# Optimization experiments

Hardware: AMD Instinct MI355X
Metric: run time of the kernel (lower is better)

The kernel has to match this reference:

```python
import jax, jax.numpy as jnp
import numpy as np
from jax import lax

T, B = 256, 64
VOCAB, EMB, HID, NLAB = 100000, 300, 256, 20
PAD_WORD = 0


def setup_inputs() -> dict:
    key = jax.random.key(0)
    ks = jax.random.split(key, 16)
    sentences = jax.random.randint(ks[0], (T, B), 0, VOCAB)
    sentences = sentences.at[0].set(jnp.maximum(sentences[0], 1))  # mask[0] must be all on (torchcrf)
    labels = jax.random.randint(ks[1], (T, B), 0, NLAB)
    s = 0.05
    emb = jax.random.normal(ks[2], (VOCAB, EMB), jnp.float32) * s
    Wih_f = jax.random.normal(ks[3], (4 * HID, EMB), jnp.float32) * s
    Whh_f = jax.random.normal(ks[4], (4 * HID, HID), jnp.float32) * s
    b_f = jax.random.normal(ks[5], (4 * HID,), jnp.float32) * s
    Wih_b = jax.random.normal(ks[6], (4 * HID, EMB), jnp.float32) * s
    Whh_b = jax.random.normal(ks[7], (4 * HID, HID), jnp.float32) * s
    b_b = jax.random.normal(ks[8], (4 * HID,), jnp.float32) * s
    W_top = jax.random.normal(ks[9], (NLAB, 2 * HID), jnp.float32) * s
    b_top = jax.random.normal(ks[10], (NLAB,), jnp.float32) * s
    start_t = jax.random.normal(ks[11], (NLAB,), jnp.float32) * 0.1
    end_t = jax.random.normal(ks[12], (NLAB,), jnp.float32) * 0.1
    trans = jax.random.normal(ks[13], (NLAB, NLAB), jnp.float32) * 0.1
    return dict(emb=emb, Wih_f=Wih_f, Whh_f=Whh_f, b_f=b_f, Wih_b=Wih_b,
                Whh_b=Whh_b, b_b=b_b, W_top=W_top, b_top=b_top,
                start_t=start_t, end_t=end_t, trans=trans,
                sentences=sentences, labels=labels)


def _lstm_dir(x, W_ih, W_hh, b, reverse):
    # x: (T, B, E) -> hs: (T, B, H); torch gate order i,f,g,o
    H = W_hh.shape[1]
    x_proj = jnp.einsum('tbe,ge->tbg', x, W_ih) + b  # precompute input projection

    def step(carry, xp):
        h, c = carry
        gates = xp + h @ W_hh.T
        i, f, g, o = jnp.split(gates, 4, axis=-1)
        c = jax.nn.sigmoid(f) * c + jax.nn.sigmoid(i) * jnp.tanh(g)
        h = jax.nn.sigmoid(o) * jnp.tanh(c)
        return (h, c), h

    init = (jnp.zeros((x.shape[1], H), x.dtype), jnp.zeros((x.shape[1], H), x.dtype))
    _, hs = lax.scan(step, init, x_proj, reverse=reverse)
    return hs


def _crf_nll(emissions, tags, mask, start_t, end_t, trans):
    # emissions: (T,B,L), tags: (T,B), mask: (T,B) bool. torchcrf math, reduction='sum'.
    Tn, Bn, L = emissions.shape
    maskf = mask.astype(emissions.dtype)
    barange = jnp.arange(Bn)
    # numerator
    score = start_t[tags[0]] + emissions[0, barange, tags[0]]
    trans_sc = trans[tags[:-1], tags[1:]]  # (T-1, B)
    emit_sc = jnp.take_along_axis(emissions[1:], tags[1:, :, None], axis=2)[..., 0]
    score = score + ((trans_sc + emit_sc) * maskf[1:]).sum(0)
    seq_ends = mask.astype(jnp.int32).sum(0) - 1  # (B,)
    last_tags = jnp.take_along_axis(tags, seq_ends[None, :], axis=0)[0]
    score = score + end_t[last_tags]
    # partition (log-sum-exp forward recurrence)
    alpha0 = start_t[None, :] + emissions[0]  # (B, L)

    def step(alpha, inp):
        emis_t, m_t = inp
        nxt = jax.nn.logsumexp(alpha[:, :, None] + trans[None] + emis_t[:, None, :], axis=1)
        return jnp.where(m_t[:, None], nxt, alpha), None

    alpha, _ = lax.scan(step, alpha0, (emissions[1:], mask[1:]))
    denom = jax.nn.logsumexp(alpha + end_t[None, :], axis=1)
    llh = (score - denom).sum()
    return -llh


def reference(emb, Wih_f, Whh_f, b_f, Wih_b, Whh_b, b_b, W_top, b_top,
              start_t, end_t, trans, sentences, labels):
    x = emb[sentences]  # (T, B, E)
    h_f = _lstm_dir(x, Wih_f, Whh_f, b_f, reverse=False)
    h_b = _lstm_dir(x, Wih_b, Whh_b, b_b, reverse=True)
    rnn_out = jnp.concatenate([h_f, h_b], axis=-1)  # (T, B, 2H)
    emissions = jnp.einsum('tbh,lh->tbl', rnn_out, W_top) + b_top
    mask = sentences != PAD_WORD
    return _crf_nll(emissions, labels, mask, start_t, end_t, trans)
```

## Files before the change

### kernel.cpp

```cpp
#include <hip/hip_runtime.h>
#include <hip/hip_bf16.h>

#define T_    256
#define B_    64
#define EMB_  300
#define HID_  256
#define G_    1024
#define L_    20
#define M_    (T_*B_)

#define NCL   32
#define CLB   8
#define BPC   4
#define UPB   32

typedef float f32x4 __attribute__((ext_vector_type(4)));
typedef unsigned long long u64;

__global__ __launch_bounds__(256) void k_xproj(
    const float* __restrict__ emb,
    const float* __restrict__ Wih_f, const float* __restrict__ b_f,
    const float* __restrict__ Wih_b, const float* __restrict__ b_b,
    const int*   __restrict__ sent,
    float* __restrict__ xp)
{
    __shared__ float As[16][68];
    __shared__ float Bs[16][68];
    __shared__ int   words[64];

    const int tid = threadIdx.x;
    const int n0  = blockIdx.x * 64;
    const int m0  = blockIdx.y * 64;
    const int dir = n0 >> 10;
    const int g0  = n0 & 1023;
    const float* __restrict__ Wih  = dir ? Wih_b : Wih_f;
    const float* __restrict__ bias = dir ? b_b   : b_f;

    if (tid < 64) words[tid] = sent[m0 + tid];
    __syncthreads();

    const int r = tid >> 2;
    const int q = tid & 3;
    const float* aptr = emb + (size_t)words[r] * EMB_ + q * 4;
    const float* bptr = Wih + (size_t)(g0 + r) * EMB_ + q * 4;

    const int tx = tid & 15;
    const int ty = tid >> 4;
    float acc[4][4] = {};

    for (int k0 = 0; k0 < 304; k0 += 16) {
        const int k = k0 + q * 4;
        float4 av = make_float4(0.f, 0.f, 0.f, 0.f);
        float4 bv = make_float4(0.f, 0.f, 0.f, 0.f);
        if (k < 300) {
            av = *(const float4*)(aptr + k0);
            bv = *(const float4*)(bptr + k0);
        }
        As[q*4+0][r] = av.x; As[q*4+1][r] = av.y; As[q*4+2][r] = av.z; As[q*4+3][r] = av.w;
        Bs[q*4+0][r] = bv.x; Bs[q*4+1][r] = bv.y; Bs[q*4+2][r] = bv.z; Bs[q*4+3][r] = bv.w;
        __syncthreads();
        #pragma unroll
        for (int kk = 0; kk < 16; ++kk) {
            const float4 a = *(const float4*)&As[kk][ty * 4];
            const float4 b = *(const float4*)&Bs[kk][tx * 4];
            acc[0][0] += a.x*b.x; acc[0][1] += a.x*b.y; acc[0][2] += a.x*b.z; acc[0][3] += a.x*b.w;
            acc[1][0] += a.y*b.x; acc[1][1] += a.y*b.y; acc[1][2] += a.y*b.z; acc[1][3] += a.y*b.w;
            acc[2][0] += a.z*b.x; acc[2][1] += a.z*b.y; acc[2][2] += a.z*b.z; acc[2][3] += a.z*b.w;
            acc[3][0] += a.w*b.x; acc[3][1] += a.w*b.y; acc[3][2] += a.w*b.z; acc[3][3] += a.w*b.w;
        }
        __syncthreads();
    }

    float* out = xp + (size_t)dir * M_ * G_;
    const int g = g0 + tx * 4;
    const float4 bs4 = *(const float4*)(bias + g);
    #pragma unroll
    for (int im = 0; im < 4; ++im) {
        const int m = m0 + ty * 4 + im;
        float4 rv;
        rv.x = acc[im][0] + bs4.x;
        rv.y = acc[im][1] + bs4.y;
        rv.z = acc[im][2] + bs4.z;
        rv.w = acc[im][3] + bs4.w;
        *(float4*)(out + (size_t)m * G_ + g) = rv;
    }
}

__global__ __launch_bounds__(256, 1) void k_lstm_scan(
    const float* __restrict__ Whh_f, const float* __restrict__ Whh_b,
    const float* __restrict__ xp, float* __restrict__ hbuf,
    u64* __restrict__ xch)
{
    const int rank = blockIdx.x & 7;
    const int cl   = blockIdx.x >> 3;
    const int dir  = cl >> 4;
    const int bg   = cl & 15;
    const int b0   = bg * BPC;
    const int u0   = rank * UPB;
    const int tid  = threadIdx.x;
    const int lane = tid & 63;
    const int w    = tid >> 6;
    const int kh   = lane & 1;
    const int g    = (lane >> 1) & 3;
    const int u_loc = (w << 3) | (lane >> 3);

    const float* __restrict__ Whh = dir ? Whh_b : Whh_f;
    const float* __restrict__ xpd = xp + (size_t)dir * M_ * G_;
    float* __restrict__ hdir = hbuf + (size_t)dir * M_ * HID_;
    u64* __restrict__ xc = xch + (size_t)cl * 2048;

    __shared__ float hs[2][BPC][264];

    for (int i = tid; i < BPC * 264; i += 256) ((float*)hs[0])[i] = 0.f;

    f32x4 wv[32];
    {
        const f32x4* wrow = (const f32x4*)(Whh + (size_t)(g * HID_ + u0 + u_loc) * HID_ + kh * 128);
        #pragma unroll
        for (int i = 0; i < 32; ++i) wv[i] = wrow[i];
    }
    __syncthreads();

    float c_reg = 0.f;
    u64 vv[4] = {0ull, 0ull, 0ull, 0ull};

    for (int t = 0; t < T_; ++t) {
        const int t_eff = dir ? (T_ - 1 - t) : t;

        #pragma unroll
        for (int i = 0; i < 32; ++i) asm volatile("" : "+v"(wv[i]));

        float x0 = 0.f, x1 = 0.f, x2 = 0.f, x3 = 0.f;
        if (kh == 0) {
            const float* xrow = xpd + ((size_t)t_eff * B_ + (b0 + g)) * G_ + (u0 + u_loc);
            x0 = xrow[0]; x1 = xrow[HID_]; x2 = xrow[2 * HID_]; x3 = xrow[3 * HID_];
        }

        u64* const slot_cur = xc + (size_t)(t & 1) * 1024;
        u64* const slot_nxt = xc + (size_t)((t + 1) & 1) * 1024;
        float* const hcur = (float*)hs[t & 1];

        #pragma unroll
        for (int b = 0; b < 4; ++b) {
            {
                const int wn = (b + 2) & 3;
                u64* const sp = (b >= 2) ? slot_nxt : slot_cur;
                vv[wn] = __hip_atomic_load(&sp[(size_t)wn * 256 + tid],
                                           __ATOMIC_RELAXED, __HIP_MEMORY_SCOPE_AGENT);
            }

            if (t > 0) {
                const unsigned want = (unsigned)t;
                u64 v = vv[b];
                while ((unsigned)(v >> 32) != want)
                    v = __hip_atomic_load(&slot_cur[(size_t)b * 256 + tid],
                                          __ATOMIC_RELAXED, __HIP_MEMORY_SCOPE_AGENT);
                hcur[b * 264 + (tid >> 7) * 132 + (tid & 127)] =
                    __uint_as_float((unsigned)v);
            }
            __syncthreads();

            const f32x4* hv = (const f32x4*)(hcur + b * 264 + kh * 132);
            float acc = 0.f;
            #pragma unroll
            for (int i = 0; i < 32; ++i) {
                const f32x4 w4 = wv[i];
                const f32x4 h4 = hv[i];
                acc += w4.x * h4.x + w4.y * h4.y + w4.z * h4.z + w4.w * h4.w;
            }
            acc += __shfl_xor(acc, 1);

            const float v1 = __shfl_xor(acc, 2);
            const float v2 = __shfl_xor(acc, 4);
            const float v3 = __shfl_xor(v1, 4);

            if (g == b && kh == 0) {
                const float arr[4] = {acc, v1, v2, v3};
                const float gi = arr[b ^ 0] + x0;
                const float gf = arr[b ^ 1] + x1;
                const float gg = arr[b ^ 2] + x2;
                const float go = arr[b ^ 3] + x3;
                const float i_ = 1.f / (1.f + __expf(-gi));
                const float f_ = 1.f / (1.f + __expf(-gf));
                const float g_ = tanhf(gg);
                const float o_ = 1.f / (1.f + __expf(-go));
                const float cn = f_ * c_reg + i_ * g_;
                const float hn = o_ * tanhf(cn);
                c_reg = cn;
                if (t + 1 < T_) {
                    const u64 pkv = ((u64)(unsigned)(t + 1) << 32) | __float_as_uint(hn);
                    __hip_atomic_store(&slot_nxt[(size_t)b * 256 + (u0 + u_loc)], pkv,
                                       __ATOMIC_RELAXED, __HIP_MEMORY_SCOPE_AGENT);
                }
                hdir[((size_t)t_eff * B_ + (b0 + b)) * HID_ + (u0 + u_loc)] = hn;
            }
        }
    }
}

__global__ __launch_bounds__(256) void k_emis(
    const float* __restrict__ Wt, const float* __restrict__ bt,
    const float* __restrict__ hbuf, float* __restrict__ em)
{
    const int gid = blockIdx.x * 256 + threadIdx.x;
    if (gid >= M_ * L_) return;
    const int m = gid / L_;
    const int l = gid - m * L_;
    const float4* hf  = (const float4*)(hbuf + (size_t)m * HID_);
    const float4* hbk = (const float4*)(hbuf + (size_t)M_ * HID_ + (size_t)m * HID_);
    const float4* w0  = (const float4*)(Wt + (size_t)l * 2 * HID_);
    const float4* w1  = w0 + HID_ / 4;
    float acc = bt[l];
    #pragma unroll 4
    for (int k = 0; k < HID_ / 4; ++k) {
        float4 h = hf[k],  w = w0[k];
        acc += h.x*w.x + h.y*w.y + h.z*w.z + h.w*w.w;
        h = hbk[k]; w = w1[k];
        acc += h.x*w.x + h.y*w.y + h.z*w.z + h.w*w.w;
    }
    em[gid] = acc;
}

__global__ __launch_bounds__(64) void k_crf(
    const float* __restrict__ start_t, const float* __restrict__ end_t,
    const float* __restrict__ trans,
    const int* __restrict__ sent, const int* __restrict__ labels,
    const float* __restrict__ em, float* __restrict__ res)
{
    const int b = blockIdx.x;
    const int tid = threadIdx.x;
    __shared__ float tr[L_ * L_];
    __shared__ float alpha[2][L_];
    __shared__ float red[64];
    __shared__ int   redi[64];
    __shared__ float sdenom;

    for (int i = tid; i < L_ * L_; i += 64) tr[i] = trans[i];
    if (tid < L_) alpha[0][tid] = start_t[tid] + em[b * L_ + tid];
    __syncthreads();

    float pre_em = (tid < L_) ? em[(B_ + b) * L_ + tid] : 0.f;
    int   pre_m  = sent[B_ + b];

    int p = 0;
    for (int t = 1; t < T_; ++t) {
        const float emt = pre_em;
        const int   mt  = pre_m;
        if (t + 1 < T_) {
            if (tid < L_) pre_em = em[((t + 1) * B_ + b) * L_ + tid];
            pre_m = sent[(t + 1) * B_ + b];
        }
        float val = 0.f;
        if (tid < L_) {
            if (mt != 0) {
                float mx = -1e30f;
                #pragma unroll
                for (int i = 0; i < L_; ++i) mx = fmaxf(mx, alpha[p][i] + tr[i * L_ + tid]);
                float s = 0.f;
                #pragma unroll
                for (int i = 0; i < L_; ++i) s += __expf(alpha[p][i] + tr[i * L_ + tid] - mx);
                val = mx + __logf(s) + emt;
            } else {
                val = alpha[p][tid];
            }
        }
        if (tid < L_) alpha[1 - p][tid] = val;
        __syncthreads();
        p ^= 1;
    }

    if (tid == 0) {
        float mx = -1e30f;
        for (int j = 0; j < L_; ++j) mx = fmaxf(mx, alpha[p][j] + end_t[j]);
        float s = 0.f;
        for (int j = 0; j < L_; ++j) s += __expf(alpha[p][j] + end_t[j] - mx);
        sdenom = mx + __logf(s);
    }

    float loc = 0.f;
    int   cnt = 0;
    for (int t = tid; t < T_; t += 64) {
        const int masked = (sent[t * B_ + b] != 0);
        cnt += masked;
        if (t >= 1 && masked) {
            const int tp = labels[(t - 1) * B_ + b];
            const int tc = labels[t * B_ + b];
            loc += tr[tp * L_ + tc] + em[(t * B_ + b) * L_ + tc];
        }
    }
    red[tid] = loc; redi[tid] = cnt;
    __syncthreads();
    if (tid == 0) {
        float s = 0.f; int c = 0;
        for (int i = 0; i < 64; ++i) { s += red[i]; c += redi[i]; }
        const int tag0 = labels[b];
        const int seq_end = c - 1;
        const int last = labels[seq_end * B_ + b];
        const float score = start_t[tag0] + em[b * L_ + tag0] + s + end_t[last];
        res[b] = score - sdenom;
    }
}

__global__ __launch_bounds__(64) void k_final(const float* __restrict__ res,
                                              float* __restrict__ out)
{
    __shared__ float red[64];
    red[threadIdx.x] = res[threadIdx.x];
    __syncthreads();
    if (threadIdx.x == 0) {
        float s = 0.f;
        for (int i = 0; i < 64; ++i) s += red[i];
        out[0] = -s;
    }
}

extern "C" void kernel_launch(void* const* d_in, const int* in_sizes, int n_in,
                              void* d_out, int out_size, void* d_ws, size_t ws_size,
                              hipStream_t stream)
{
    const float* emb     = (const float*)d_in[0];
    const float* Wih_f   = (const float*)d_in[1];
    const float* Whh_f   = (const float*)d_in[2];
    const float* b_f     = (const float*)d_in[3];
    const float* Wih_b   = (const float*)d_in[4];
    const float* Whh_b   = (const float*)d_in[5];
    const float* b_b     = (const float*)d_in[6];
    const float* W_top   = (const float*)d_in[7];
    const float* b_top   = (const float*)d_in[8];
    const float* start_t = (const float*)d_in[9];
    const float* end_t   = (const float*)d_in[10];
    const float* trans   = (const float*)d_in[11];
    const int*   sent    = (const int*)d_in[12];
    const int*   labels  = (const int*)d_in[13];
    float* out = (float*)d_out;

    float* wsf  = (float*)d_ws;
    float* xp   = wsf;
    float* hbuf = xp   + (size_t)2 * M_ * G_;
    float* em   = hbuf + (size_t)2 * M_ * HID_;
    float* res  = em   + (size_t)M_ * L_;
    u64*   xch  = (u64*)(res + 64);

    k_xproj<<<dim3(2048 / 64, M_ / 64), 256, 0, stream>>>(
        emb, Wih_f, b_f, Wih_b, b_b, sent, xp);

    {
        void* args[] = { (void*)&Whh_f, (void*)&Whh_b, (void*)&xp, (void*)&hbuf, (void*)&xch };
        hipLaunchCooperativeKernel((const void*)k_lstm_scan, dim3(256), dim3(256),
                                   args, 0, stream);
    }

    k_emis<<<(M_ * L_ + 255) / 256, 256, 0, stream>>>(W_top, b_top, hbuf, em);

    k_crf<<<B_, 64, 0, stream>>>(start_t, end_t, trans, sent, labels, em, res);

    k_final<<<1, 64, 0, stream>>>(res, out);
}
```

Before: 2.093 ms.

## Interleave two batch groups per LSTM block to hide cross-block exchange latency

Each scan block now handles two independent batch groups (A and B) and alternates between them. While it waits for the peers' hidden-state exchange for one group, it computes the other group, and it prefetches the exchange slots and input projections one phase ahead. The per-batch sync is replaced with one sync per group and a transpose-shuffle gate reduction, and the grid is halved to 128 blocks. The intent is to hide spin-wait latency on the sequential recurrence, at the cost of using half the CUs and doing twice the serial compute per block.

```diff
diff --git a/kernel.cpp b/kernel.cpp
--- a/kernel.cpp
+++ b/kernel.cpp
@@ -9,8 +9,6 @@
 #define L_    20
 #define M_    (T_*B_)
 
-#define NCL   32
-#define CLB   8
 #define BPC   4
 #define UPB   32
 
@@ -92,26 +90,34 @@
     u64* __restrict__ xch)
 {
     const int rank = blockIdx.x & 7;
-    const int cl   = blockIdx.x >> 3;
-    const int dir  = cl >> 4;
-    const int bg   = cl & 15;
-    const int b0   = bg * BPC;
+    const int mcl  = blockIdx.x >> 3;
+    const int dir  = mcl >> 3;
+    const int bp   = mcl & 7;
+    const int b0A  = (bp * 2) * BPC;
+    const int b0B  = b0A + BPC;
     const int u0   = rank * UPB;
     const int tid  = threadIdx.x;
     const int lane = tid & 63;
     const int w    = tid >> 6;
     const int kh   = lane & 1;
+    const int gb0  = (lane >> 1) & 1;
+    const int gb1  = (lane >> 2) & 1;
     const int g    = (lane >> 1) & 3;
     const int u_loc = (w << 3) | (lane >> 3);
 
     const float* __restrict__ Whh = dir ? Whh_b : Whh_f;
     const float* __restrict__ xpd = xp + (size_t)dir * M_ * G_;
     float* __restrict__ hdir = hbuf + (size_t)dir * M_ * HID_;
-    u64* __restrict__ xc = xch + (size_t)cl * 2048;
-
-    __shared__ float hs[2][BPC][264];
-
-    for (int i = tid; i < BPC * 264; i += 256) ((float*)hs[0])[i] = 0.f;
+    u64* __restrict__ xcA = xch + (size_t)(dir * 16 + bp * 2) * 2048;
+    u64* __restrict__ xcB = xcA + 2048;
+
+    __shared__ float hsA[2][BPC][264];
+    __shared__ float hsB[2][BPC][264];
+
+    for (int i = tid; i < 2 * BPC * 264; i += 256) {
+        ((float*)hsA)[i] = 0.f;
+        ((float*)hsB)[i] = 0.f;
+    }
 
     f32x4 wv[32];
     {
@@ -121,81 +127,130 @@
     }
     __syncthreads();
 
-    float c_reg = 0.f;
-    u64 vv[4] = {0ull, 0ull, 0ull, 0ull};
+    float cA = 0.f, cB = 0.f;
+    u64 vvA[4] = {0ull, 0ull, 0ull, 0ull};
+    u64 vvB[4] = {0ull, 0ull, 0ull, 0ull};
+    const int act = (kh == 0);
+
+    float xA0 = 0.f, xA1 = 0.f, xA2 = 0.f, xA3 = 0.f;
+    float xB0 = 0.f, xB1 = 0.f, xB2 = 0.f, xB3 = 0.f;
+    if (act) {
+        const int te0 = dir ? (T_ - 1) : 0;
+        const float* xrow = xpd + ((size_t)te0 * B_ + (b0A + g)) * G_ + (u0 + u_loc);
+        xA0 = xrow[0]; xA1 = xrow[HID_]; xA2 = xrow[2 * HID_]; xA3 = xrow[3 * HID_];
+    }
+
+    #define SPIN_FILL(VV, XC, HS, T)                                              \
+        {                                                                         \
+            const unsigned want = (unsigned)(T);                                  \
+            u64* const sl = (XC) + (size_t)((T) & 1) * 1024;                      \
+            u64 v[4] = {VV[0], VV[1], VV[2], VV[3]};                              \
+            while ((unsigned)(v[0] >> 32) != want || (unsigned)(v[1] >> 32) != want || \
+                   (unsigned)(v[2] >> 32) != want || (unsigned)(v[3] >> 32) != want) { \
+                _Pragma("unroll")                                                 \
+                for (int i = 0; i < 4; ++i)                                       \
+                    if ((unsigned)(v[i] >> 32) != want)                           \
+                        v[i] = __hip_atomic_load(&sl[(size_t)i * 256 + tid],      \
+                                 __ATOMIC_RELAXED, __HIP_MEMORY_SCOPE_AGENT);     \
+            }                                                                     \
+            float* hw = (float*)(HS)[(T) & 1];                                    \
+            _Pragma("unroll")                                                     \
+            for (int i = 0; i < 4; ++i)                                           \
+                hw[i * 264 + ((tid >> 7) * 132) + (tid & 127)] =                  \
+                    __uint_as_float((unsigned)v[i]);                              \
+        }
+
+    #define PHASE_COMPUTE(HS, T, TEFF, X0, X1, X2, X3, CREG, XC, B0)              \
+        {                                                                         \
+            float a[4];                                                           \
+            _Pragma("unroll")                                                     \
+            for (int b = 0; b < BPC; ++b) {                                       \
+                const f32x4* hv = (const f32x4*)((const float*)(HS)[(T) & 1] + b * 264 + kh * 132); \
+                float acc = 0.f;                                                  \
+                _Pragma("unroll")                                                 \
+                for (int i = 0; i < 32; ++i) {                                    \
+                    const f32x4 w4 = wv[i];                                       \
+                    const f32x4 h4 = hv[i];                                       \
+                    acc += w4.x * h4.x + w4.y * h4.y + w4.z * h4.z + w4.w * h4.w; \
+                }                                                                 \
+                acc += __shfl_xor(acc, 1);                                        \
+                a[b] = acc;                                                       \
+            }                                                                     \
+            const float s01 = gb0 ? a[0] : a[1];                                  \
+            const float r01 = __shfl_xor(s01, 2);                                 \
+            const float n0 = gb0 ? r01 : a[0];                                    \
+            const float n1 = gb0 ? a[1] : r01;                                    \
+            const float s23 = gb0 ? a[2] : a[3];                                  \
+            const float r23 = __shfl_xor(s23, 2);                                 \
+            const float n2 = gb0 ? r23 : a[2];                                    \
+            const float n3 = gb0 ? a[3] : r23;                                    \
+            const float s02 = gb1 ? n0 : n2;                                      \
+            const float r02 = __shfl_xor(s02, 4);                                 \
+            const float p0 = gb1 ? r02 : n0;                                      \
+            const float p2 = gb1 ? n2 : r02;                                      \
+            const float s13 = gb1 ? n1 : n3;                                      \
+            const float r13 = __shfl_xor(s13, 4);                                 \
+            const float p1 = gb1 ? r13 : n1;                                      \
+            const float p3 = gb1 ? n3 : r13;                                      \
+            if (act) {                                                            \
+                const float gi = p0 + (X0);                                       \
+                const float gf = p1 + (X1);                                       \
+                const float gg = p2 + (X2);                                       \
+                const float go = p3 + (X3);                                       \
+                const float i_ = 1.f / (1.f + __expf(-gi));                       \
+                const float f_ = 1.f / (1.f + __expf(-gf));                       \
+                const float g_ = tanhf(gg);                                       \
+                const float o_ = 1.f / (1.f + __expf(-go));                       \
+                const float cn = f_ * (CREG) + i_ * g_;                           \
+                const float hn = o_ * tanhf(cn);                                  \
+                (CREG) = cn;                                                      \
+                if ((T) + 1 < T_) {                                               \
+                    const u64 pkv = ((u64)(unsigned)((T) + 1) << 32) | __float_as_uint(hn); \
+                    __hip_atomic_store(&(XC)[(size_t)(((T) + 1) & 1) * 1024 + (size_t)g * 256 + (u0 + u_loc)], \
+                                       pkv, __ATOMIC_RELAXED, __HIP_MEMORY_SCOPE_AGENT); \
+                }                                                                 \
+                hdir[((size_t)(TEFF) * B_ + ((B0) + g)) * HID_ + (u0 + u_loc)] = hn; \
+            }                                                                     \
+        }
 
     for (int t = 0; t < T_; ++t) {
-        const int t_eff = dir ? (T_ - 1 - t) : t;
+        const int t_eff  = dir ? (T_ - 1 - t) : t;
+        const int tn     = (t + 1 < T_) ? (t + 1) : (T_ - 1);
+        const int tn_eff = dir ? (T_ - 1 - tn) : tn;
 
         #pragma unroll
         for (int i = 0; i < 32; ++i) asm volatile("" : "+v"(wv[i]));
 
-        float x0 = 0.f, x1 = 0.f, x2 = 0.f, x3 = 0.f;
-        if (kh == 0) {
-            const float* xrow = xpd + ((size_t)t_eff * B_ + (b0 + g)) * G_ + (u0 + u_loc);
-            x0 = xrow[0]; x1 = xrow[HID_]; x2 = xrow[2 * HID_]; x3 = xrow[3 * HID_];
-        }
-
-        u64* const slot_cur = xc + (size_t)(t & 1) * 1024;
-        u64* const slot_nxt = xc + (size_t)((t + 1) & 1) * 1024;
-        float* const hcur = (float*)hs[t & 1];
+        if (t > 0) SPIN_FILL(vvA, xcA, hsA, t);
+        __syncthreads();
 
         #pragma unroll
-        for (int b = 0; b < 4; ++b) {
-            {
-                const int wn = (b + 2) & 3;
-                u64* const sp = (b >= 2) ? slot_nxt : slot_cur;
-                vv[wn] = __hip_atomic_load(&sp[(size_t)wn * 256 + tid],
-                                           __ATOMIC_RELAXED, __HIP_MEMORY_SCOPE_AGENT);
-            }
-
-            if (t > 0) {
-                const unsigned want = (unsigned)t;
-                u64 v = vv[b];
-                while ((unsigned)(v >> 32) != want)
-                    v = __hip_atomic_load(&slot_cur[(size_t)b * 256 + tid],
-                                          __ATOMIC_RELAXED, __HIP_MEMORY_SCOPE_AGENT);
-                hcur[b * 264 + (tid >> 7) * 132 + (tid & 127)] =
-                    __uint_as_float((unsigned)v);
-            }
-            __syncthreads();
-
-            const f32x4* hv = (const f32x4*)(hcur + b * 264 + kh * 132);
-            float acc = 0.f;
-            #pragma unroll
-            for (int i = 0; i < 32; ++i) {
-                const f32x4 w4 = wv[i];
-                const f32x4 h4 = hv[i];
-                acc += w4.x * h4.x + w4.y * h4.y + w4.z * h4.z + w4.w * h4.w;
-            }
-            acc += __shfl_xor(acc, 1);
-
-            const float v1 = __shfl_xor(acc, 2);
-            const float v2 = __shfl_xor(acc, 4);
-            const float v3 = __shfl_xor(v1, 4);
-
-            if (g == b && kh == 0) {
-                const float arr[4] = {acc, v1, v2, v3};
-                const float gi = arr[b ^ 0] + x0;
-                const float gf = arr[b ^ 1] + x1;
-                const float gg = arr[b ^ 2] + x2;
-                const float go = arr[b ^ 3] + x3;
-                const float i_ = 1.f / (1.f + __expf(-gi));
-                const float f_ = 1.f / (1.f + __expf(-gf));
-                const float g_ = tanhf(gg);
-                const float o_ = 1.f / (1.f + __expf(-go));
-                const float cn = f_ * c_reg + i_ * g_;
-                const float hn = o_ * tanhf(cn);
-                c_reg = cn;
-                if (t + 1 < T_) {
-                    const u64 pkv = ((u64)(unsigned)(t + 1) << 32) | __float_as_uint(hn);
-                    __hip_atomic_store(&slot_nxt[(size_t)b * 256 + (u0 + u_loc)], pkv,
+        for (int i = 0; i < 4; ++i)
+            vvB[i] = __hip_atomic_load(&xcB[(size_t)(t & 1) * 1024 + (size_t)i * 256 + tid],
                                        __ATOMIC_RELAXED, __HIP_MEMORY_SCOPE_AGENT);
-                }
-                hdir[((size_t)t_eff * B_ + (b0 + b)) * HID_ + (u0 + u_loc)] = hn;
-            }
-        }
-    }
+        if (act) {
+            const float* xrow = xpd + ((size_t)t_eff * B_ + (b0B + g)) * G_ + (u0 + u_loc);
+            xB0 = xrow[0]; xB1 = xrow[HID_]; xB2 = xrow[2 * HID_]; xB3 = xrow[3 * HID_];
+        }
+
+        PHASE_COMPUTE(hsA, t, t_eff, xA0, xA1, xA2, xA3, cA, xcA, b0A);
+
+        if (t > 0) SPIN_FILL(vvB, xcB, hsB, t);
+        __syncthreads();
+
+        #pragma unroll
+        for (int i = 0; i < 4; ++i)
+            vvA[i] = __hip_atomic_load(&xcA[(size_t)((t + 1) & 1) * 1024 + (size_t)i * 256 + tid],
+                                       __ATOMIC_RELAXED, __HIP_MEMORY_SCOPE_AGENT);
+        if (act) {
+            const float* xrow = xpd + ((size_t)tn_eff * B_ + (b0A + g)) * G_ + (u0 + u_loc);
+            xA0 = xrow[0]; xA1 = xrow[HID_]; xA2 = xrow[2 * HID_]; xA3 = xrow[3 * HID_];
+        }
+
+        PHASE_COMPUTE(hsB, t, t_eff, xB0, xB1, xB2, xB3, cB, xcB, b0B);
+    }
+    #undef SPIN_FILL
+    #undef PHASE_COMPUTE
 }
 
 __global__ __launch_bounds__(256) void k_emis(
@@ -346,7 +401,7 @@
 
     {
         void* args[] = { (void*)&Whh_f, (void*)&Whh_b, (void*)&xp, (void*)&hbuf, (void*)&xch };
-        hipLaunchCooperativeKernel((const void*)k_lstm_scan, dim3(256), dim3(256),
+        hipLaunchCooperativeKernel((const void*)k_lstm_scan, dim3(128), dim3(256),
                                    args, 0, stream);
     }
 
```

New measurement: 2.481 ms. 1.19x slower.
